# Kernel tuning notes

Hardware: AMD Instinct MI355X
Metric: run time of the kernel (lower is better)

The kernel has to match this reference:

```python
import jax, jax.numpy as jnp
import numpy as np

D_MODEL = 1024
N_HEADS = 16
D_HEAD = D_MODEL // N_HEADS
B, T = 4, 1024


def rotate_half(x):
    # interleaved rotate: (x0,x1,x2,x3,...) -> (-x1,x0,-x3,x2,...)
    x_even = x[..., ::2]
    x_odd = x[..., 1::2]
    return jnp.stack((-x_odd, x_even), axis=-1).reshape(x.shape)


def apply_rope(x, cos, sin):
    return x * cos + rotate_half(x) * sin


def setup_inputs() -> dict:
    key = jax.random.key(0)
    k1, k2, k3, k4, k5 = jax.random.split(key, 5)
    x = jax.random.normal(k1, (B, T, D_MODEL), dtype=jnp.float32)
    rope_cos = jax.random.normal(k2, (1, 1, T, D_HEAD), dtype=jnp.float32)
    rope_sin = jax.random.normal(k3, (1, 1, T, D_HEAD), dtype=jnp.float32)
    Wqkv = jax.random.normal(k4, (D_MODEL, 3 * D_MODEL), dtype=jnp.float32) * (D_MODEL ** -0.5)
    Wproj = jax.random.normal(k5, (D_MODEL, D_MODEL), dtype=jnp.float32) * (D_MODEL ** -0.5)
    return {"x": x, "rope_cos": rope_cos, "rope_sin": rope_sin, "Wqkv": Wqkv, "Wproj": Wproj}


def reference(x, rope_cos, rope_sin, Wqkv, Wproj):
    b, t, _ = x.shape
    qkv = x @ Wqkv  # [b, t, 3*d_model]
    q, k, v = jnp.split(qkv, 3, axis=-1)
    # [b, h, t, d_head]
    q = q.reshape(b, t, N_HEADS, D_HEAD).transpose(0, 2, 1, 3)
    k = k.reshape(b, t, N_HEADS, D_HEAD).transpose(0, 2, 1, 3)
    v = v.reshape(b, t, N_HEADS, D_HEAD).transpose(0, 2, 1, 3)
    q = apply_rope(q, rope_cos, rope_sin)
    k = apply_rope(k, rope_cos, rope_sin)
    scale = 1.0 / jnp.sqrt(jnp.asarray(D_HEAD, dtype=q.dtype))
    scores = jnp.einsum('bhqd,bhkd->bhqk', q, k) * scale
    causal = jnp.tril(jnp.ones((t, t), dtype=bool))
    scores = jnp.where(causal, scores, jnp.asarray(-jnp.inf, dtype=scores.dtype))
    attn = jax.nn.softmax(scores, axis=-1)
    out = jnp.einsum('bhqk,bhkd->bhqd', attn, v)
    out = out.transpose(0, 2, 1, 3).reshape(b, t, D_MODEL)
    return out @ Wproj
```

## Files before the change

### kernel.cpp

```cpp
#include <hip/hip_runtime.h>
#include <hip/hip_bf16.h>
#include <math.h>

#define SEQ_T   1024
#define DMODEL  1024
#define NHEAD   16
#define DHEAD   64
#define MROWS   4096
#define QKV_N   3072

typedef __attribute__((ext_vector_type(8))) short  short8;
typedef __attribute__((ext_vector_type(4))) float  f32x4;
typedef __attribute__((ext_vector_type(4))) unsigned short us4;

__device__ __forceinline__ unsigned short f2bf(float f) {
    unsigned u = __float_as_uint(f);
    u += 0x7FFF + ((u >> 16) & 1);
    return (unsigned short)(u >> 16);
}
__device__ __forceinline__ float bf2f(unsigned short u) {
    return __uint_as_float((unsigned)u << 16);
}

__device__ __forceinline__ void gload_lds16(const void* g, void* lds) {
    __builtin_amdgcn_global_load_lds(
        (const __attribute__((address_space(1))) void*)g,
        (__attribute__((address_space(3))) void*)lds, 16, 0, 0);
}

__global__ __launch_bounds__(256) void k_prep(
    const float* __restrict__ x, const float* __restrict__ wqkv,
    const float* __restrict__ wproj,
    unsigned short* __restrict__ xbf, unsigned short* __restrict__ wqkvt,
    unsigned short* __restrict__ wprojt)
{
    __shared__ float t[32][33];
    const int bid = blockIdx.x;
    const int tid = threadIdx.x;

    if (bid < 2048) {
        const int f = bid * 256 + tid;
        const float4 a = ((const float4*)x)[f * 2];
        const float4 b = ((const float4*)x)[f * 2 + 1];
        short8 o;
        o[0] = (short)f2bf(a.x); o[1] = (short)f2bf(a.y);
        o[2] = (short)f2bf(a.z); o[3] = (short)f2bf(a.w);
        o[4] = (short)f2bf(b.x); o[5] = (short)f2bf(b.y);
        o[6] = (short)f2bf(b.z); o[7] = (short)f2bf(b.w);
        *(short8*)&xbf[f * 8] = o;
        return;
    }

    const float* in;
    unsigned short* out;
    int N, tt;
    if (bid < 5120) { in = wqkv;  out = wqkvt;  N = QKV_N; tt = bid - 2048; }
    else            { in = wproj; out = wprojt; N = 1024;  tt = bid - 5120; }
    const int ntx = N / 32;
    const int N0 = (tt % ntx) * 32, K0 = (tt / ntx) * 32;

    const int row = tid >> 3, c4 = (tid & 7) * 4;
    const float4 v = *(const float4*)&in[(size_t)(K0 + row) * N + N0 + c4];
    t[c4 + 0][row] = v.x; t[c4 + 1][row] = v.y;
    t[c4 + 2][row] = v.z; t[c4 + 3][row] = v.w;
    __syncthreads();
    us4 o;
    o[0] = f2bf(t[row][c4 + 0]); o[1] = f2bf(t[row][c4 + 1]);
    o[2] = f2bf(t[row][c4 + 2]); o[3] = f2bf(t[row][c4 + 3]);
    *(us4*)&out[(size_t)(N0 + row) * 1024 + K0 + c4] = o;
}

__device__ __forceinline__ void gemm_mainloop(
    const unsigned short* __restrict__ A, const unsigned short* __restrict__ Bt,
    int M0, int N0, unsigned short* As, unsigned short* Bs, f32x4 acc[4][4])
{
    const int tid  = threadIdx.x;
    const int lane = tid & 63, wave = tid >> 6;
    const int wr = wave >> 1, wc = wave & 1;
    const int l15 = lane & 15, l4 = lane >> 4;

    for (int kt = 0; kt < 1024; kt += 32) {
        __syncthreads();
        #pragma unroll
        for (int is = 0; is < 2; is++) {
            const int f = is * 256 + tid;
            const int row = f >> 2, seg = f & 3;
            gload_lds16(A  + (size_t)(M0 + row) * 1024 + kt + seg * 8,
                        (char*)As + is * 4096 + wave * 1024);
            gload_lds16(Bt + (size_t)(N0 + row) * 1024 + kt + seg * 8,
                        (char*)Bs + is * 4096 + wave * 1024);
        }
        __syncthreads();

        short8 af[4], bfr[4];
        #pragma unroll
        for (int m = 0; m < 4; m++)
            af[m] = *(const short8*)((const char*)As +
                     ((wr * 64 + m * 16 + l15) * 64 + l4 * 16));
        #pragma unroll
        for (int n = 0; n < 4; n++)
            bfr[n] = *(const short8*)((const char*)Bs +
                     ((wc * 64 + n * 16 + l15) * 64 + l4 * 16));
        #pragma unroll
        for (int m = 0; m < 4; m++)
            #pragma unroll
            for (int n = 0; n < 4; n++)
                acc[m][n] = __builtin_amdgcn_mfma_f32_16x16x32_bf16(
                    af[m], bfr[n], acc[m][n], 0, 0, 0);
    }
}

__global__ __launch_bounds__(256) void k_gemm_qkv(
    const unsigned short* __restrict__ Xbf, const unsigned short* __restrict__ Wt,
    const float* __restrict__ COS, const float* __restrict__ SIN,
    unsigned short* __restrict__ qws, unsigned short* __restrict__ kws,
    unsigned short* __restrict__ vws)
{
    __shared__ __align__(16) unsigned short As[4096];
    __shared__ __align__(16) unsigned short Bs[4096];
    const int M0 = blockIdx.y * 128, N0 = blockIdx.x * 128;

    f32x4 acc[4][4];
    #pragma unroll
    for (int m = 0; m < 4; m++)
        #pragma unroll
        for (int n = 0; n < 4; n++) acc[m][n] = (f32x4)0.f;

    gemm_mainloop(Xbf, Wt, M0, N0, As, Bs, acc);

    const int tid  = threadIdx.x;
    const int lane = tid & 63, wave = tid >> 6;
    const int wr = wave >> 1, wc = wave & 1;
    const int l15 = lane & 15, l4 = lane >> 4;
    const int which = N0 >> 10;

    if (which == 2) {
        #pragma unroll
        for (int m = 0; m < 4; m++) {
            const int rowbase = M0 + wr * 64 + m * 16 + l4 * 4;
            const int bb = rowbase >> 10, t0 = rowbase & 1023;
            #pragma unroll
            for (int n = 0; n < 4; n++) {
                const int cin = (N0 + wc * 64 + n * 16) & 1023;
                const int hh = cin >> 6, d = (cin & 63) + l15;
                us4 o4;
                #pragma unroll
                for (int r = 0; r < 4; r++) o4[r] = f2bf(acc[m][n][r]);
                *(us4*)&vws[(((size_t)bb * NHEAD + hh) * DHEAD + d) * SEQ_T + t0] = o4;
            }
        }
    } else {
        unsigned short* dst = (which == 0) ? qws : kws;
        #pragma unroll
        for (int m = 0; m < 4; m++) {
            #pragma unroll
            for (int n = 0; n < 4; n++) {
                const int cin = (N0 + wc * 64 + n * 16) & 1023;
                const int hh = cin >> 6;
                const int d = (cin & 63) + l15;
                const int rowbase = M0 + wr * 64 + m * 16 + l4 * 4;
                #pragma unroll
                for (int r = 0; r < 4; r++) {
                    const int row = rowbase + r;
                    const int bb = row >> 10, t = row & 1023;
                    const float v = acc[m][n][r];
                    const float p = __shfl_xor(v, 1, 64);
                    const float c = COS[t * 64 + d];
                    const float s = SIN[t * 64 + d];
                    float o = (lane & 1) ? fmaf(v, c, p * s) : fmaf(v, c, -(p * s));
                    if (which == 0) o *= 0.125f;
                    dst[(((size_t)bb * NHEAD + hh) * SEQ_T + t) * DHEAD + d] = f2bf(o);
                }
            }
        }
    }
}

__global__ __launch_bounds__(256) void k_gemm_proj(
    const unsigned short* __restrict__ Abf, const unsigned short* __restrict__ Wt,
    float* __restrict__ C)
{
    __shared__ __align__(16) unsigned short As[4096];
    __shared__ __align__(16) unsigned short Bs[4096];
    const int M0 = blockIdx.y * 128, N0 = blockIdx.x * 128;

    f32x4 acc[4][4];
    #pragma unroll
    for (int m = 0; m < 4; m++)
        #pragma unroll
        for (int n = 0; n < 4; n++) acc[m][n] = (f32x4)0.f;

    gemm_mainloop(Abf, Wt, M0, N0, As, Bs, acc);

    const int tid  = threadIdx.x;
    const int lane = tid & 63, wave = tid >> 6;
    const int wr = wave >> 1, wc = wave & 1;
    const int l15 = lane & 15, l4 = lane >> 4;

    #pragma unroll
    for (int m = 0; m < 4; m++) {
        #pragma unroll
        for (int n = 0; n < 4; n++) {
            const int col = N0 + wc * 64 + n * 16 + l15;
            const int rowbase = M0 + wr * 64 + m * 16 + l4 * 4;
            #pragma unroll
            for (int r = 0; r < 4; r++)
                C[(size_t)(rowbase + r) * 1024 + col] = acc[m][n][r];
        }
    }
}

__global__ __launch_bounds__(256) void k_attn(
    const unsigned short* __restrict__ qg, const unsigned short* __restrict__ kg,
    const unsigned short* __restrict__ vtg, unsigned short* __restrict__ og)
{
    __shared__ __align__(16) unsigned short Ks[2][4096];
    __shared__ __align__(16) unsigned short Vts[2][4096];
    __shared__ __align__(16) unsigned short Ps[8][1024];

    const int tid  = threadIdx.x;
    const int lane = tid & 63, w = tid >> 6;
    const int l15 = lane & 15, l4 = lane >> 4, l7 = lane & 7;

    const int logical = (blockIdx.x & 7) * 64 + (blockIdx.x >> 3);
    const int bh = logical >> 3, pair = logical & 7;
    const int b = bh >> 4, h = bh & 15;
    const int qtA = pair, qtB = 15 - pair;

    const size_t hb     = (size_t)b * NHEAD + h;
    const size_t qkbase = hb * SEQ_T * DHEAD;
    const size_t vtbase = hb * DHEAD * SEQ_T;

    const int qrowA = qtA * 64 + w * 16 + l15;
    const int qrowB = qtB * 64 + w * 16 + l15;
    const short8 aqA0 = *(const short8*)&qg[qkbase + (size_t)qrowA * 64 +      l4 * 8];
    const short8 aqA1 = *(const short8*)&qg[qkbase + (size_t)qrowA * 64 + 32 + l4 * 8];
    const short8 aqB0 = *(const short8*)&qg[qkbase + (size_t)qrowB * 64 +      l4 * 8];
    const short8 aqB1 = *(const short8*)&qg[qkbase + (size_t)qrowB * 64 + 32 + l4 * 8];

    f32x4 OA[4], OB[4];
    float mA[4], lA[4], mB[4], lB[4];
    #pragma unroll
    for (int nd = 0; nd < 4; nd++) { OA[nd] = (f32x4)0.f; OB[nd] = (f32x4)0.f; }
    #pragma unroll
    for (int r = 0; r < 4; r++) {
        mA[r] = -INFINITY; lA[r] = 0.f; mB[r] = -INFINITY; lB[r] = 0.f;
    }

    auto STAGE = [&](int jt, int bi) {
        #pragma unroll
        for (int i = 0; i < 2; i++) {
            const int c = i * 256 + tid;
            const int row = c >> 3, ps = c & 7;
            const int ls = ps ^ (row & 7);
            gload_lds16(kg + qkbase + (size_t)(jt * 64 + row) * 64 + ls * 8,
                        (char*)&Ks[bi][0] + i * 4096 + w * 1024);
            gload_lds16(vtg + vtbase + (size_t)row * 1024 + jt * 64 + ls * 8,
                        (char*)&Vts[bi][0] + i * 4096 + w * 1024);
        }
    };

    auto STRIP = [&](const short8& aq0, const short8& aq1, f32x4* O,
                     float* m_i, float* l_i, unsigned short* pw,
                     const unsigned short* Kb, const unsigned short* Vb,
                     bool maskdiag) {
        f32x4 S[4];
        #pragma unroll
        for (int n = 0; n < 4; n++) S[n] = (f32x4)0.f;
        __builtin_amdgcn_s_setprio(1);
        #pragma unroll
        for (int n = 0; n < 4; n++) {
            const int krow = n * 16 + l15;
            const short8 bk0 = *(const short8*)((const char*)Kb +
                                krow * 128 + (((0 + l4) ^ l7) << 4));
            const short8 bk1 = *(const short8*)((const char*)Kb +
                                krow * 128 + (((4 + l4) ^ l7) << 4));
            S[n] = __builtin_amdgcn_mfma_f32_16x16x32_bf16(aq0, bk0, S[n], 0, 0, 0);
            S[n] = __builtin_amdgcn_mfma_f32_16x16x32_bf16(aq1, bk1, S[n], 0, 0, 0);
        }
        __builtin_amdgcn_s_setprio(0);
        if (maskdiag) {
            #pragma unroll
            for (int n = 0; n < 4; n++)
                #pragma unroll
                for (int r = 0; r < 4; r++)
                    if (n * 16 + l15 > w * 16 + l4 * 4 + r) S[n][r] = -INFINITY;
        }
        #pragma unroll
        for (int r = 0; r < 4; r++) {
            float mx = fmaxf(fmaxf(S[0][r], S[1][r]), fmaxf(S[2][r], S[3][r]));
            #pragma unroll
            for (int off = 1; off < 16; off <<= 1)
                mx = fmaxf(mx, __shfl_xor(mx, off, 64));
            const float mnew  = fmaxf(m_i[r], mx);
            const float alpha = __expf(m_i[r] - mnew);
            m_i[r] = mnew;
            float rs = 0.f;
            #pragma unroll
            for (int n = 0; n < 4; n++) {
                const float p = __expf(S[n][r] - mnew);
                S[n][r] = p;
                rs += p;
            }
            #pragma unroll
            for (int off = 1; off < 16; off <<= 1)
                rs += __shfl_xor(rs, off, 64);
            l_i[r] = l_i[r] * alpha + rs;
            #pragma unroll
            for (int nd = 0; nd < 4; nd++) O[nd][r] *= alpha;
        }
        #pragma unroll
        for (int n = 0; n < 4; n++)
            #pragma unroll
            for (int r = 0; r < 4; r++) {
                const int q = l4 * 4 + r;
                const int byteoff = q * 128 + ((n * 32 + l15 * 2) ^ ((q & 7) << 4));
                *(unsigned short*)((char*)pw + byteoff) = f2bf(S[n][r]);
            }
        const short8 pa0 = *(const short8*)((const char*)pw +
                            l15 * 128 + (((0 + l4) ^ l7) << 4));
        const short8 pa1 = *(const short8*)((const char*)pw +
                            l15 * 128 + (((4 + l4) ^ l7) << 4));
        __builtin_amdgcn_s_setprio(1);
        #pragma unroll
        for (int nd = 0; nd < 4; nd++) {
            const int drow = nd * 16 + l15;
            const short8 v0 = *(const short8*)((const char*)Vb +
                               drow * 128 + (((0 + l4) ^ l7) << 4));
            const short8 v1 = *(const short8*)((const char*)Vb +
                               drow * 128 + (((4 + l4) ^ l7) << 4));
            O[nd] = __builtin_amdgcn_mfma_f32_16x16x32_bf16(pa0, v0, O[nd], 0, 0, 0);
            O[nd] = __builtin_amdgcn_mfma_f32_16x16x32_bf16(pa1, v1, O[nd], 0, 0, 0);
        }
        __builtin_amdgcn_s_setprio(0);
    };

    const int nt = qtB + 1;
    STAGE(0, 0);
    __syncthreads();

    for (int jt = 0; jt < nt; ++jt) {
        const int cur = jt & 1;
        if (jt + 1 < nt) STAGE(jt + 1, cur ^ 1);
        STRIP(aqB0, aqB1, OB, mB, lB, &Ps[w * 2 + 1][0],
              &Ks[cur][0], &Vts[cur][0], jt == qtB);
        if (jt <= qtA)
            STRIP(aqA0, aqA1, OA, mA, lA, &Ps[w * 2 + 0][0],
                  &Ks[cur][0], &Vts[cur][0], jt == qtA);
        __syncthreads();
    }

    #pragma unroll
    for (int r = 0; r < 4; r++) {
        const float invA = 1.0f / lA[r];
        const float invB = 1.0f / lB[r];
        const int tqA = qtA * 64 + w * 16 + l4 * 4 + r;
        const int tqB = qtB * 64 + w * 16 + l4 * 4 + r;
        #pragma unroll
        for (int nd = 0; nd < 4; nd++) {
            const int d = nd * 16 + l15;
            og[((size_t)b * SEQ_T + tqA) * DMODEL + h * 64 + d] = f2bf(OA[nd][r] * invA);
            og[((size_t)b * SEQ_T + tqB) * DMODEL + h * 64 + d] = f2bf(OB[nd][r] * invB);
        }
    }
}

extern "C" void kernel_launch(void* const* d_in, const int* in_sizes, int n_in,
                              void* d_out, int out_size, void* d_ws, size_t ws_size,
                              hipStream_t stream)
{
    const float* x     = (const float*)d_in[0];
    const float* cosb  = (const float*)d_in[1];
    const float* sinb  = (const float*)d_in[2];
    const float* wqkv  = (const float*)d_in[3];
    const float* wproj = (const float*)d_in[4];
    float* out = (float*)d_out;

    char* ws = (char*)d_ws;
    unsigned short* qbf    = (unsigned short*)(ws);
    unsigned short* kbf    = (unsigned short*)(ws + (8u<<20));
    unsigned short* vtbf   = (unsigned short*)(ws + (16u<<20));
    unsigned short* xbf    = (unsigned short*)(ws + (24u<<20));
    unsigned short* wqkvt  = (unsigned short*)(ws + (32u<<20));
    unsigned short* wprojt = (unsigned short*)(ws + (38u<<20));
    unsigned short* awsbf  = (unsigned short*)(ws + (40u<<20));

    k_prep<<<6144, 256, 0, stream>>>(x, wqkv, wproj, xbf, wqkvt, wprojt);
    k_gemm_qkv<<<dim3(QKV_N / 128, MROWS / 128), 256, 0, stream>>>(
        xbf, wqkvt, cosb, sinb, qbf, kbf, vtbf);
    k_attn<<<512, 256, 0, stream>>>(qbf, kbf, vtbf, awsbf);
    k_gemm_proj<<<dim3(DMODEL / 128, MROWS / 128), 256, 0, stream>>>(awsbf, wprojt, out);
}
```

Before: 194.7 us.

## Widen GEMM K-step to 64 with XOR-swizzled LDS and XCD-aware tile mapping

The shared GEMM mainloop now stages 64-wide K slices instead of 32, which halves the barrier count per tile, and stores them with an XOR swizzle on 16-byte segments to avoid LDS bank conflicts on the fragment reads. Both GEMM kernels switch to a 1D grid whose block ids are remapped so that blocks on the same XCD work on neighbouring M/N tiles, aiming for better L2 reuse of A and B. LDS use per block doubles, which may lower occupancy.

```diff
diff --git a/kernel.cpp b/kernel.cpp
--- a/kernel.cpp
+++ b/kernel.cpp
@@ -79,34 +79,42 @@
     const int wr = wave >> 1, wc = wave & 1;
     const int l15 = lane & 15, l4 = lane >> 4;
 
-    for (int kt = 0; kt < 1024; kt += 32) {
+    for (int kt = 0; kt < 1024; kt += 64) {
         __syncthreads();
         #pragma unroll
-        for (int is = 0; is < 2; is++) {
+        for (int is = 0; is < 4; is++) {
             const int f = is * 256 + tid;
-            const int row = f >> 2, seg = f & 3;
-            gload_lds16(A  + (size_t)(M0 + row) * 1024 + kt + seg * 8,
+            const int row = f >> 3, ps = f & 7;
+            const int ls = ps ^ (row & 7);
+            gload_lds16(A  + (size_t)(M0 + row) * 1024 + kt + ls * 8,
                         (char*)As + is * 4096 + wave * 1024);
-            gload_lds16(Bt + (size_t)(N0 + row) * 1024 + kt + seg * 8,
+            gload_lds16(Bt + (size_t)(N0 + row) * 1024 + kt + ls * 8,
                         (char*)Bs + is * 4096 + wave * 1024);
         }
         __syncthreads();
 
-        short8 af[4], bfr[4];
-        #pragma unroll
-        for (int m = 0; m < 4; m++)
-            af[m] = *(const short8*)((const char*)As +
-                     ((wr * 64 + m * 16 + l15) * 64 + l4 * 16));
-        #pragma unroll
-        for (int n = 0; n < 4; n++)
-            bfr[n] = *(const short8*)((const char*)Bs +
-                     ((wc * 64 + n * 16 + l15) * 64 + l4 * 16));
-        #pragma unroll
-        for (int m = 0; m < 4; m++)
-            #pragma unroll
-            for (int n = 0; n < 4; n++)
-                acc[m][n] = __builtin_amdgcn_mfma_f32_16x16x32_bf16(
-                    af[m], bfr[n], acc[m][n], 0, 0, 0);
+        #pragma unroll
+        for (int kk = 0; kk < 2; kk++) {
+            short8 af[4], bfr[4];
+            #pragma unroll
+            for (int m = 0; m < 4; m++) {
+                const int row = wr * 64 + m * 16 + l15;
+                const int slot = (kk * 4 + l4) ^ (row & 7);
+                af[m] = *(const short8*)((const char*)As + row * 128 + slot * 16);
+            }
+            #pragma unroll
+            for (int n = 0; n < 4; n++) {
+                const int row = wc * 64 + n * 16 + l15;
+                const int slot = (kk * 4 + l4) ^ (row & 7);
+                bfr[n] = *(const short8*)((const char*)Bs + row * 128 + slot * 16);
+            }
+            #pragma unroll
+            for (int m = 0; m < 4; m++)
+                #pragma unroll
+                for (int n = 0; n < 4; n++)
+                    acc[m][n] = __builtin_amdgcn_mfma_f32_16x16x32_bf16(
+                        af[m], bfr[n], acc[m][n], 0, 0, 0);
+        }
     }
 }
 
@@ -116,9 +124,17 @@
     unsigned short* __restrict__ qws, unsigned short* __restrict__ kws,
     unsigned short* __restrict__ vws)
 {
-    __shared__ __align__(16) unsigned short As[4096];
-    __shared__ __align__(16) unsigned short Bs[4096];
-    const int M0 = blockIdx.y * 128, N0 = blockIdx.x * 128;
+    __shared__ __align__(16) unsigned short As[8192];
+    __shared__ __align__(16) unsigned short Bs[8192];
+
+    const int bid = blockIdx.x;
+    const int xcd = bid & 7, idx = bid >> 3;
+    const int chunk = idx >> 5, within = idx & 31;
+    const int wm = within >> 2, wn = within & 3;
+    const int chunk_id = xcd + 8 * chunk;
+    const int cm = chunk_id & 3, cn = chunk_id >> 2;
+    const int M0 = (cm * 8 + wm) * 128;
+    const int N0 = (cn * 4 + wn) * 128;
 
     f32x4 acc[4][4];
     #pragma unroll
@@ -180,9 +196,15 @@
     const unsigned short* __restrict__ Abf, const unsigned short* __restrict__ Wt,
     float* __restrict__ C)
 {
-    __shared__ __align__(16) unsigned short As[4096];
-    __shared__ __align__(16) unsigned short Bs[4096];
-    const int M0 = blockIdx.y * 128, N0 = blockIdx.x * 128;
+    __shared__ __align__(16) unsigned short As[8192];
+    __shared__ __align__(16) unsigned short Bs[8192];
+
+    const int bid = blockIdx.x;
+    const int xcd = bid & 7, idx = bid >> 3;
+    const int wm = idx >> 2, wn = idx & 3;
+    const int cm = xcd & 3, cn = xcd >> 2;
+    const int M0 = (cm * 8 + wm) * 128;
+    const int N0 = (cn * 4 + wn) * 128;
 
     f32x4 acc[4][4];
     #pragma unroll
@@ -386,8 +408,7 @@
     unsigned short* awsbf  = (unsigned short*)(ws + (40u<<20));
 
     k_prep<<<6144, 256, 0, stream>>>(x, wqkv, wproj, xbf, wqkvt, wprojt);
-    k_gemm_qkv<<<dim3(QKV_N / 128, MROWS / 128), 256, 0, stream>>>(
-        xbf, wqkvt, cosb, sinb, qbf, kbf, vtbf);
+    k_gemm_qkv<<<768, 256, 0, stream>>>(xbf, wqkvt, cosb, sinb, qbf, kbf, vtbf);
     k_attn<<<512, 256, 0, stream>>>(qbf, kbf, vtbf, awsbf);
-    k_gemm_proj<<<dim3(DMODEL / 128, MROWS / 128), 256, 0, stream>>>(awsbf, wprojt, out);
-}
+    k_gemm_proj<<<256, 256, 0, stream>>>(awsbf, wprojt, out);
+}
```

After: 187.3 us. 1.04x faster.
